# Performance work log

Hardware: AMD Instinct MI355X
Metric: run time of the kernel (lower is better)

The kernel has to match this reference:

```python
import jax, jax.numpy as jnp
import numpy as np

F = 128          # feature_size
C = 300          # n_content_dims
V = 100001       # n_nodes + 1 (embedding rows)
N0, N1, N2 = 409600, 40960, 4096   # NodeFlow layer sizes (fanout ~10)
E0, E1 = 409600, 40960             # edges in block0 (L0->L1) and block1 (L1->L2)


def setup_inputs() -> dict:
    key = jax.random.key(0)
    ks = jax.random.split(key, 24)
    std = 1.0 / F
    xav_p = float(np.sqrt(6.0 / (C + F)))   # xavier_uniform for proj Linear(C->F)
    xav_c = float(np.sqrt(6.0 / (2 * F + F)))  # xavier_uniform for conv Linear(2F->F)
    return {
        'nid0': jax.random.randint(ks[0], (N0,), 0, 100000),
        'nid1': jax.random.randint(ks[1], (N1,), 0, 100000),
        'nid2': jax.random.randint(ks[2], (N2,), 0, 100000),
        'content0': jax.random.normal(ks[3], (N0, C), jnp.float32),
        'content1': jax.random.normal(ks[4], (N1, C), jnp.float32),
        'content2': jax.random.normal(ks[5], (N2, C), jnp.float32),
        'block0_src': jax.random.randint(ks[6], (E0,), 0, N0),
        'block0_dst': jax.random.randint(ks[7], (E0,), 0, N1),
        'block1_src': jax.random.randint(ks[8], (E1,), 0, N1),
        'block1_dst': jax.random.randint(ks[9], (E1,), 0, N2),
        'node_emb': jax.random.normal(ks[10], (V, F), jnp.float32) * std,
        'Wp0': jax.random.uniform(ks[11], (F, C), jnp.float32, -xav_p, xav_p),
        'bp0': jnp.zeros((F,), jnp.float32),
        'Wp1': jax.random.uniform(ks[12], (F, C), jnp.float32, -xav_p, xav_p),
        'bp1': jnp.zeros((F,), jnp.float32),
        'Wp2': jax.random.uniform(ks[13], (F, C), jnp.float32, -xav_p, xav_p),
        'bp2': jnp.zeros((F,), jnp.float32),
        'Wc0': jax.random.uniform(ks[14], (F, 2 * F), jnp.float32, -xav_c, xav_c),
        'bc0': jnp.zeros((F,), jnp.float32),
        'Wc1': jax.random.uniform(ks[15], (F, 2 * F), jnp.float32, -xav_c, xav_c),
        'bc1': jnp.zeros((F,), jnp.float32),
    }


def _embed(node_emb, nid, content, Wp, bp):
    # h = node_emb(nid + 1) + LeakyReLU(content @ Wp.T + bp)   (dropout is eval no-op)
    return node_emb[nid + 1] + jax.nn.leaky_relu(content @ Wp.T + bp)


def _conv(h_src, src, dst, h_self, n_dst, W, b):
    # DGL block_compute: copy_src('h')+sum -> h_agg ; copy_src('one')+sum -> w
    msgs = h_src[src]                                    # [E, F] gather
    h_agg = jax.ops.segment_sum(msgs, dst, num_segments=n_dst)
    w = jax.ops.segment_sum(jnp.ones((src.shape[0],), h_src.dtype), dst,
                            num_segments=n_dst)
    h_agg = (h_agg - h_self) / jnp.maximum(w - 1.0, 1.0)[:, None]
    h_new = jax.nn.leaky_relu(jnp.concatenate([h_self, h_agg], axis=1) @ W.T + b)
    nrm = jnp.maximum(jnp.linalg.norm(h_new, axis=1, keepdims=True), 1e-6)
    return h_new / nrm


def reference(nid0, nid1, nid2, content0, content1, content2,
              block0_src, block0_dst, block1_src, block1_dst,
              node_emb, Wp0, bp0, Wp1, bp1, Wp2, bp2,
              Wc0, bc0, Wc1, bc1):
    h0 = _embed(node_emb, nid0, content0, Wp0, bp0)   # [N0, F]
    h1 = _embed(node_emb, nid1, content1, Wp1, bp1)   # [N1, F]
    h2 = _embed(node_emb, nid2, content2, Wp2, bp2)   # [N2, F]
    h1 = _conv(h0, block0_src, block0_dst, h1, N1, Wc0, bc0)
    h2 = _conv(h1, block1_src, block1_dst, h2, N2, Wc1, bc1)
    return h2
```

## Files before the change

kernel.cpp:

```cpp
#include <hip/hip_runtime.h>
#include <hip/hip_bf16.h>
#include <math.h>

#define F 128
#define C 300
#define CKP 320
#define NKT 10
#define K2F 256
#define N0_ 409600
#define N1_ 40960
#define N2_ 4096
#define E0_ 409600
#define E1_ 40960
#define CAP 64
#define LDA 40

typedef unsigned short u16;
typedef unsigned int u32;
typedef __attribute__((ext_vector_type(8))) short short8;
typedef __attribute__((ext_vector_type(8))) unsigned short u16x8;
typedef __attribute__((ext_vector_type(4))) float f32x4;

__device__ __forceinline__ float lrelu(float x) { return x > 0.f ? x : 0.01f * x; }

__device__ __forceinline__ u16 f2bf(float x) {
  __hip_bfloat16 h = __float2bfloat16(x);
  u16 r; __builtin_memcpy(&r, &h, 2); return r;
}
__device__ __forceinline__ float bf2f(u16 v) {
  union { u32 u; float f; } c; c.u = ((u32)v) << 16; return c.f;
}

#define GLOAD_LDS16(gp, lp) \
  __builtin_amdgcn_global_load_lds( \
      (const __attribute__((address_space(1))) void*)(const void*)(gp), \
      (__attribute__((address_space(3))) void*)(lp), 16, 0, 0)

__global__ __launch_bounds__(256) void zero_kernel(float4* __restrict__ p, int n4) {
  int i = blockIdx.x * 256 + threadIdx.x;
  if (i < n4) p[i] = make_float4(0.f, 0.f, 0.f, 0.f);
}

__global__ __launch_bounds__(256) void convert_all(
    const float* __restrict__ Wp0, const float* __restrict__ Wp1,
    const float* __restrict__ Wp2, const float* __restrict__ Wc0,
    const float* __restrict__ Wc1,
    u16* __restrict__ Wpb0, u16* __restrict__ Wpb1, u16* __restrict__ Wpb2,
    u16* __restrict__ Wcb0, u16* __restrict__ Wcb1)
{
  int i = blockIdx.x * 256 + threadIdx.x;
  const int P = F * CKP, Q = F * K2F;
  const float* W; u16* O; int K, KP, j;
  if      (i < P)         { W = Wp0; O = Wpb0; K = C;   KP = CKP; j = i; }
  else if (i < 2 * P)     { W = Wp1; O = Wpb1; K = C;   KP = CKP; j = i - P; }
  else if (i < 3 * P)     { W = Wp2; O = Wpb2; K = C;   KP = CKP; j = i - 2 * P; }
  else if (i < 3 * P + Q) { W = Wc0; O = Wcb0; K = K2F; KP = K2F; j = i - 3 * P; }
  else if (i < 3 * P + 2 * Q) { W = Wc1; O = Wcb1; K = K2F; KP = K2F; j = i - 3 * P - Q; }
  else return;
  int f = j / KP, k = j - f * KP;
  O[j] = (k < K) ? f2bf(W[(size_t)f * K + k]) : (u16)0;
}

__global__ __launch_bounds__(256) void build_csr(
    const int* __restrict__ b0s, const int* __restrict__ b0d,
    const int* __restrict__ b1s, const int* __restrict__ b1d,
    int* __restrict__ deg0, int* __restrict__ deg1,
    int* __restrict__ csr0, int* __restrict__ csr1)
{
  int e = blockIdx.x * 256 + threadIdx.x;
  if (e < E0_) {
    int d = b0d[e];
    int slot = atomicAdd(&deg0[d], 1);
    if (slot < CAP) csr0[(size_t)d * CAP + slot] = b0s[e];
  } else {
    int e1 = e - E0_;
    if (e1 < E1_) {
      int d = b1d[e1];
      int slot = atomicAdd(&deg1[d], 1);
      if (slot < CAP) csr1[(size_t)d * CAP + slot] = b1s[e1];
    }
  }
}

struct Afrag { float4 x00, x01, x10, x11; };

__global__ __launch_bounds__(256, 2) void embed_all(
    const float* __restrict__ content0, const float* __restrict__ content1,
    const float* __restrict__ content2,
    const u16* __restrict__ Wpb0, const u16* __restrict__ Wpb1,
    const u16* __restrict__ Wpb2,
    const float* __restrict__ bp0, const float* __restrict__ bp1,
    const float* __restrict__ bp2,
    const int* __restrict__ nid0, const int* __restrict__ nid1,
    const int* __restrict__ nid2,
    const float* __restrict__ emb,
    u16* __restrict__ out0, u16* __restrict__ out1, u16* __restrict__ out2)
{
  __shared__ u16 Bs[NKT * 128 * 32];
  const int t = threadIdx.x, lane = t & 63, w = t >> 6;
  const int b = blockIdx.x;

  const float* content; const u16* Wpb; const float* bp; const int* nid;
  u16* out; int ostride, row0;
  if (b < N0_ / 128) {
    content = content0; Wpb = Wpb0; bp = bp0; nid = nid0;
    out = out0; ostride = F; row0 = b * 128;
  } else if (b < N0_ / 128 + N1_ / 128) {
    content = content1; Wpb = Wpb1; bp = bp1; nid = nid1;
    out = out1; ostride = 2 * F; row0 = (b - N0_ / 128) * 128;
  } else {
    content = content2; Wpb = Wpb2; bp = bp2; nid = nid2;
    out = out2; ostride = 2 * F; row0 = (b - N0_ / 128 - N1_ / 128) * 128;
  }

  {
    const int j_in = lane >> 2, u_in = lane & 3;
#pragma unroll
    for (int cc = 0; cc < 20; ++cc) {
      int c = w * 20 + cc;
      int kt = c >> 3, j0 = (c & 7) * 16;
      int j = j0 + j_in;
      int u = u_in ^ (j & 3);
      const u16* gp = Wpb + (size_t)j * CKP + kt * 32 + u * 8;
      GLOAD_LDS16(gp, &Bs[(size_t)(kt * 128 + j0) * 32]);
    }
  }

  f32x4 acc[2][8];
#pragma unroll
  for (int fr = 0; fr < 2; ++fr)
#pragma unroll
    for (int fc = 0; fc < 8; ++fc) {
      acc[fr][fc][0] = 0.f; acc[fr][fc][1] = 0.f;
      acc[fr][fc][2] = 0.f; acc[fr][fc][3] = 0.f;
    }

  const int frow = lane & 15, g = lane >> 4;
  const float* c0p = content + (size_t)(row0 + w * 32 + frow) * C;
  const float* c1p = c0p + (size_t)16 * C;

  auto loadA = [&](int kt) -> Afrag {
    Afrag r;
    int col = kt * 32 + g * 8;
    if (kt < NKT - 1) {
      r.x00 = *(const float4*)(c0p + col); r.x01 = *(const float4*)(c0p + col + 4);
      r.x10 = *(const float4*)(c1p + col); r.x11 = *(const float4*)(c1p + col + 4);
    } else {
      float v0[8], v1[8];
#pragma unroll
      for (int i = 0; i < 8; ++i) {
        int cc = col + i;
        v0[i] = (cc < C) ? c0p[cc] : 0.f;
        v1[i] = (cc < C) ? c1p[cc] : 0.f;
      }
      r.x00 = make_float4(v0[0], v0[1], v0[2], v0[3]);
      r.x01 = make_float4(v0[4], v0[5], v0[6], v0[7]);
      r.x10 = make_float4(v1[0], v1[1], v1[2], v1[3]);
      r.x11 = make_float4(v1[4], v1[5], v1[6], v1[7]);
    }
    return r;
  };

  const int bsw = (g ^ (frow & 3)) * 8;
  auto compute = [&](const Afrag& a, int kt) {
    u16x8 a0v, a1v;
    a0v[0]=f2bf(a.x00.x); a0v[1]=f2bf(a.x00.y); a0v[2]=f2bf(a.x00.z); a0v[3]=f2bf(a.x00.w);
    a0v[4]=f2bf(a.x01.x); a0v[5]=f2bf(a.x01.y); a0v[6]=f2bf(a.x01.z); a0v[7]=f2bf(a.x01.w);
    a1v[0]=f2bf(a.x10.x); a1v[1]=f2bf(a.x10.y); a1v[2]=f2bf(a.x10.z); a1v[3]=f2bf(a.x10.w);
    a1v[4]=f2bf(a.x11.x); a1v[5]=f2bf(a.x11.y); a1v[6]=f2bf(a.x11.z); a1v[7]=f2bf(a.x11.w);
    short8 a0 = *(short8*)&a0v, a1 = *(short8*)&a1v;
#pragma unroll
    for (int fc = 0; fc < 8; ++fc) {
      short8 bfr = *(const short8*)&Bs[(size_t)(kt * 128 + fc * 16 + frow) * 32 + bsw];
      acc[0][fc] = __builtin_amdgcn_mfma_f32_16x16x32_bf16(a0, bfr, acc[0][fc], 0, 0, 0);
      acc[1][fc] = __builtin_amdgcn_mfma_f32_16x16x32_bf16(a1, bfr, acc[1][fc], 0, 0, 0);
    }
  };

  Afrag A0 = loadA(0);
  Afrag A1 = loadA(1);
  __syncthreads();
  Afrag A2 = loadA(2); compute(A0, 0);
  Afrag A3 = loadA(3); compute(A1, 1);
  A0 = loadA(4);       compute(A2, 2);
  A1 = loadA(5);       compute(A3, 3);
  A2 = loadA(6);       compute(A0, 4);
  A3 = loadA(7);       compute(A1, 5);
  A0 = loadA(8);       compute(A2, 6);
  A1 = loadA(9);       compute(A3, 7);
  compute(A0, 8);
  compute(A1, 9);

  float bpv[8];
#pragma unroll
  for (int fc = 0; fc < 8; ++fc) bpv[fc] = bp[fc * 16 + frow];
#pragma unroll
  for (int fr = 0; fr < 2; ++fr) {
#pragma unroll
    for (int q = 0; q < 4; ++q) {
      int n = row0 + w * 32 + fr * 16 + g * 4 + q;
      int gi = nid[n] + 1;
      const float* erow = emb + (size_t)gi * F;
      u16* orow = out + (size_t)n * ostride;
#pragma unroll
      for (int fc = 0; fc < 8; ++fc) {
        int col = fc * 16 + frow;
        float v = acc[fr][fc][q] + bpv[fc];
        orow[col] = f2bf(erow[col] + lrelu(v));
      }
    }
  }
}

__global__ __launch_bounds__(256) void gather_xa(
    const u16* __restrict__ hsrc, const int* __restrict__ csr,
    const int* __restrict__ deg, u16* __restrict__ xcat)
{
  int d = blockIdx.x * 4 + (threadIdx.x >> 6);
  int lane = threadIdx.x & 63;
  u32 hv = *(const u32*)&xcat[(size_t)d * (2 * F) + lane * 2];
  float h0f = bf2f((u16)(hv & 0xffff)), h1f = bf2f((u16)(hv >> 16));
  int dg = deg[d];
  int n = dg < CAP ? dg : CAP;
  const int* cp = csr + (size_t)d * CAP;
  float s0 = 0.f, s1 = 0.f;
  int j = 0;
  for (; j + 4 <= n; j += 4) {
    int i0 = cp[j], i1 = cp[j + 1], i2 = cp[j + 2], i3 = cp[j + 3];
    u32 v0 = *(const u32*)&hsrc[(size_t)i0 * F + lane * 2];
    u32 v1 = *(const u32*)&hsrc[(size_t)i1 * F + lane * 2];
    u32 v2 = *(const u32*)&hsrc[(size_t)i2 * F + lane * 2];
    u32 v3 = *(const u32*)&hsrc[(size_t)i3 * F + lane * 2];
    s0 += bf2f((u16)(v0 & 0xffff)) + bf2f((u16)(v1 & 0xffff))
        + bf2f((u16)(v2 & 0xffff)) + bf2f((u16)(v3 & 0xffff));
    s1 += bf2f((u16)(v0 >> 16)) + bf2f((u16)(v1 >> 16))
        + bf2f((u16)(v2 >> 16)) + bf2f((u16)(v3 >> 16));
  }
  for (; j < n; ++j) {
    u32 v = *(const u32*)&hsrc[(size_t)cp[j] * F + lane * 2];
    s0 += bf2f((u16)(v & 0xffff));
    s1 += bf2f((u16)(v >> 16));
  }
  float inv = 1.f / fmaxf((float)dg - 1.f, 1.f);
  u16 a0 = f2bf((s0 - h0f) * inv), a1 = f2bf((s1 - h1f) * inv);
  *(u32*)&xcat[(size_t)d * (2 * F) + F + lane * 2] = ((u32)a1 << 16) | a0;
}

template<int F32OUT>
__global__ __launch_bounds__(256) void conv_mfma(
    const u16* __restrict__ xcat, const u16* __restrict__ Wcb,
    const float* __restrict__ bc, u16* __restrict__ outb,
    float* __restrict__ outf)
{
  __shared__ u16 As[128][LDA];
  __shared__ u16 Bs[128][LDA];
  const int t = threadIdx.x;
  const int lane = t & 63, w = t >> 6;
  const int row0 = blockIdx.x * 128;

  f32x4 acc[2][8];
#pragma unroll
  for (int fr = 0; fr < 2; ++fr)
#pragma unroll
    for (int fc = 0; fc < 8; ++fc) {
      acc[fr][fc][0] = 0.f; acc[fr][fc][1] = 0.f;
      acc[fr][fc][2] = 0.f; acc[fr][fc][3] = 0.f;
    }

  for (int k0 = 0; k0 < K2F; k0 += 32) {
    if (k0) __syncthreads();
#pragma unroll
    for (int it = 0; it < 2; ++it) {
      int cc = it * 256 + t;
      int r = cc >> 2, kc = (cc & 3) * 8;
      *(u16x8*)&As[r][kc] = *(const u16x8*)&xcat[(size_t)(row0 + r) * K2F + k0 + kc];
      *(u16x8*)&Bs[r][kc] = *(const u16x8*)&Wcb[(size_t)r * K2F + k0 + kc];
    }
    __syncthreads();

    const int frow = lane & 15;
    const int kc = (lane >> 4) * 8;
    short8 a0 = *(const short8*)&As[w * 32 + frow][kc];
    short8 a1 = *(const short8*)&As[w * 32 + 16 + frow][kc];
#pragma unroll
    for (int fc = 0; fc < 8; ++fc) {
      short8 b = *(const short8*)&Bs[fc * 16 + frow][kc];
      acc[0][fc] = __builtin_amdgcn_mfma_f32_16x16x32_bf16(a0, b, acc[0][fc], 0, 0, 0);
      acc[1][fc] = __builtin_amdgcn_mfma_f32_16x16x32_bf16(a1, b, acc[1][fc], 0, 0, 0);
    }
  }

  float bcv[8];
#pragma unroll
  for (int fc = 0; fc < 8; ++fc) bcv[fc] = bc[fc * 16 + (lane & 15)];
#pragma unroll
  for (int fr = 0; fr < 2; ++fr) {
#pragma unroll
    for (int q = 0; q < 4; ++q) {
      float x[8];
      float ss = 0.f;
#pragma unroll
      for (int fc = 0; fc < 8; ++fc) {
        x[fc] = lrelu(acc[fr][fc][q] + bcv[fc]);
        ss += x[fc] * x[fc];
      }
#pragma unroll
      for (int m = 8; m >= 1; m >>= 1) ss += __shfl_xor(ss, m, 64);
      float nrm = 1.f / fmaxf(sqrtf(ss), 1e-6f);
      int n = row0 + w * 32 + fr * 16 + (lane >> 4) * 4 + q;
#pragma unroll
      for (int fc = 0; fc < 8; ++fc) {
        int col = fc * 16 + (lane & 15);
        if (F32OUT) outf[(size_t)n * F + col] = x[fc] * nrm;
        else        outb[(size_t)n * F + col] = f2bf(x[fc] * nrm);
      }
    }
  }
}

extern "C" void kernel_launch(void* const* d_in, const int* in_sizes, int n_in,
                              void* d_out, int out_size, void* d_ws, size_t ws_size,
                              hipStream_t stream) {
  const int*   nid0     = (const int*)d_in[0];
  const int*   nid1     = (const int*)d_in[1];
  const int*   nid2     = (const int*)d_in[2];
  const float* content0 = (const float*)d_in[3];
  const float* content1 = (const float*)d_in[4];
  const float* content2 = (const float*)d_in[5];
  const int*   b0s      = (const int*)d_in[6];
  const int*   b0d      = (const int*)d_in[7];
  const int*   b1s      = (const int*)d_in[8];
  const int*   b1d      = (const int*)d_in[9];
  const float* emb      = (const float*)d_in[10];
  const float* Wp0      = (const float*)d_in[11];
  const float* bp0      = (const float*)d_in[12];
  const float* Wp1      = (const float*)d_in[13];
  const float* bp1      = (const float*)d_in[14];
  const float* Wp2      = (const float*)d_in[15];
  const float* bp2      = (const float*)d_in[16];
  const float* Wc0      = (const float*)d_in[17];
  const float* bc0      = (const float*)d_in[18];
  const float* Wc1      = (const float*)d_in[19];
  const float* bc1      = (const float*)d_in[20];

  u16* wsu = (u16*)d_ws;
  u16* h0b   = wsu;
  u16* xcat1 = h0b + (size_t)N0_ * F;
  u16* xcat2 = xcat1 + (size_t)N1_ * 2 * F;
  u16* h1nb  = xcat2 + (size_t)N2_ * 2 * F;
  u16* Wpb0  = h1nb + (size_t)N1_ * F;
  u16* Wpb1  = Wpb0 + (size_t)F * CKP;
  u16* Wpb2  = Wpb1 + (size_t)F * CKP;
  u16* Wcb0  = Wpb2 + (size_t)F * CKP;
  u16* Wcb1  = Wcb0 + (size_t)F * K2F;
  int* deg0  = (int*)(Wcb1 + (size_t)F * K2F);
  int* deg1  = deg0 + N1_;
  int* csr0  = deg1 + N2_;
  int* csr1  = csr0 + (size_t)N1_ * CAP;

  const int zn4 = (N1_ + N2_) / 4;
  zero_kernel<<<(zn4 + 255) / 256, 256, 0, stream>>>((float4*)deg0, zn4);

  build_csr<<<(E0_ + E1_ + 255) / 256, 256, 0, stream>>>(
      b0s, b0d, b1s, b1d, deg0, deg1, csr0, csr1);

  convert_all<<<(3 * F * CKP + 2 * F * K2F + 255) / 256, 256, 0, stream>>>(
      Wp0, Wp1, Wp2, Wc0, Wc1, Wpb0, Wpb1, Wpb2, Wcb0, Wcb1);

  embed_all<<<(N0_ + N1_ + N2_) / 128, 256, 0, stream>>>(
      content0, content1, content2, Wpb0, Wpb1, Wpb2,
      bp0, bp1, bp2, nid0, nid1, nid2, emb, h0b, xcat1, xcat2);

  gather_xa<<<N1_ / 4, 256, 0, stream>>>(h0b, csr0, deg0, xcat1);
  conv_mfma<0><<<N1_ / 128, 256, 0, stream>>>(xcat1, Wcb0, bc0, h1nb, nullptr);

  gather_xa<<<N2_ / 4, 256, 0, stream>>>(h1nb, csr1, deg1, xcat2);
  conv_mfma<1><<<N2_ / 128, 256, 0, stream>>>(xcat2, Wcb1, bc1, nullptr, (float*)d_out);
}
```

Measured before the change: 321.6 us.

## Make embed GEMM persistent with per-wave double-buffered coalesced panel loads

The embed kernel becomes a persistent grid of 256 blocks, with each wave looping over 16-row panels in strided order. Each panel is loaded with fully coalesced float4 reads of contiguous content rows into a register double buffer. It is then converted to bf16 and staged in a per-wave LDS tile before the MFMA k-loop. This loads the projection weights into LDS once per block instead of once per 128 rows and improves global read coalescing. In exchange it uses heavy register buffering (38 float4 per lane), one block per CU, and a per-wave LDS write/read round trip with no explicit wave barrier.

```diff
diff --git a/kernel.cpp b/kernel.cpp
--- a/kernel.cpp
+++ b/kernel.cpp
@@ -14,9 +14,18 @@
 #define E1_ 40960
 #define CAP 64
 #define LDA 40
+#define ALD 328
+
+#define NB0 230
+#define NB1 23
+#define NB2 3
+#define NP0 (N0_ / 16)
+#define NP1 (N1_ / 16)
+#define NP2 (N2_ / 16)
 
 typedef unsigned short u16;
 typedef unsigned int u32;
+typedef __attribute__((ext_vector_type(2))) unsigned int u32x2;
 typedef __attribute__((ext_vector_type(8))) short short8;
 typedef __attribute__((ext_vector_type(8))) unsigned short u16x8;
 typedef __attribute__((ext_vector_type(4))) float f32x4;
@@ -82,9 +91,7 @@
   }
 }
 
-struct Afrag { float4 x00, x01, x10, x11; };
-
-__global__ __launch_bounds__(256, 2) void embed_all(
+__global__ __launch_bounds__(256, 1) void embed_all(
     const float* __restrict__ content0, const float* __restrict__ content1,
     const float* __restrict__ content2,
     const u16* __restrict__ Wpb0, const u16* __restrict__ Wpb1,
@@ -97,20 +104,21 @@
     u16* __restrict__ out0, u16* __restrict__ out1, u16* __restrict__ out2)
 {
   __shared__ u16 Bs[NKT * 128 * 32];
+  __shared__ u16 As[4][16][ALD];
   const int t = threadIdx.x, lane = t & 63, w = t >> 6;
   const int b = blockIdx.x;
 
   const float* content; const u16* Wpb; const float* bp; const int* nid;
-  u16* out; int ostride, row0;
-  if (b < N0_ / 128) {
+  u16* out; int ostride, npan, wstr, bl;
+  if (b < NB0) {
     content = content0; Wpb = Wpb0; bp = bp0; nid = nid0;
-    out = out0; ostride = F; row0 = b * 128;
-  } else if (b < N0_ / 128 + N1_ / 128) {
+    out = out0; ostride = F;     npan = NP0; wstr = NB0 * 4; bl = b;
+  } else if (b < NB0 + NB1) {
     content = content1; Wpb = Wpb1; bp = bp1; nid = nid1;
-    out = out1; ostride = 2 * F; row0 = (b - N0_ / 128) * 128;
+    out = out1; ostride = 2 * F; npan = NP1; wstr = NB1 * 4; bl = b - NB0;
   } else {
     content = content2; Wpb = Wpb2; bp = bp2; nid = nid2;
-    out = out2; ostride = 2 * F; row0 = (b - N0_ / 128 - N1_ / 128) * 128;
+    out = out2; ostride = 2 * F; npan = NP2; wstr = NB2 * 4; bl = b - NB0 - NB1;
   }
 
   {
@@ -126,89 +134,91 @@
     }
   }
 
-  f32x4 acc[2][8];
-#pragma unroll
-  for (int fr = 0; fr < 2; ++fr)
+#pragma unroll
+  for (int j = 0; j < 3; ++j) {
+    int idx = j * 64 + lane;
+    if (idx < 160) {
+      int r = idx / 10, kk = 300 + (idx % 10) * 2;
+      *(u32*)&As[w][r][kk] = 0u;
+    }
+  }
+
+  const int frow = lane & 15, g = lane >> 4;
+  const int bsw = (g ^ (frow & 3)) * 8;
+  float bpv[8];
+#pragma unroll
+  for (int fc = 0; fc < 8; ++fc) bpv[fc] = bp[fc * 16 + frow];
+
+  f32x4 acc[8];
+
+  auto loadP = [&](float4* buf, int pl) {
+    const float* ab = content + (size_t)pl * 16 * C;
+#pragma unroll
+    for (int i = 0; i < 19; ++i) {
+      int c = i * 64 + lane;
+      if (c < 1200) buf[i] = *(const float4*)(ab + (size_t)c * 4);
+      else buf[i] = make_float4(0.f, 0.f, 0.f, 0.f);
+    }
+  };
+  auto cvtWrite = [&](const float4* buf) {
+#pragma unroll
+    for (int i = 0; i < 19; ++i) {
+      int c = i * 64 + lane;
+      if (c < 1200) {
+        int r = c / 75, k0 = (c % 75) * 4;
+        u32 lo = ((u32)f2bf(buf[i].y) << 16) | f2bf(buf[i].x);
+        u32 hi = ((u32)f2bf(buf[i].w) << 16) | f2bf(buf[i].z);
+        u32x2 pk; pk[0] = lo; pk[1] = hi;
+        *(u32x2*)&As[w][r][k0] = pk;
+      }
+    }
+  };
+  auto kloop = [&]() {
 #pragma unroll
     for (int fc = 0; fc < 8; ++fc) {
-      acc[fr][fc][0] = 0.f; acc[fr][fc][1] = 0.f;
-      acc[fr][fc][2] = 0.f; acc[fr][fc][3] = 0.f;
-    }
-
-  const int frow = lane & 15, g = lane >> 4;
-  const float* c0p = content + (size_t)(row0 + w * 32 + frow) * C;
-  const float* c1p = c0p + (size_t)16 * C;
-
-  auto loadA = [&](int kt) -> Afrag {
-    Afrag r;
-    int col = kt * 32 + g * 8;
-    if (kt < NKT - 1) {
-      r.x00 = *(const float4*)(c0p + col); r.x01 = *(const float4*)(c0p + col + 4);
-      r.x10 = *(const float4*)(c1p + col); r.x11 = *(const float4*)(c1p + col + 4);
-    } else {
-      float v0[8], v1[8];
-#pragma unroll
-      for (int i = 0; i < 8; ++i) {
-        int cc = col + i;
-        v0[i] = (cc < C) ? c0p[cc] : 0.f;
-        v1[i] = (cc < C) ? c1p[cc] : 0.f;
-      }
-      r.x00 = make_float4(v0[0], v0[1], v0[2], v0[3]);
-      r.x01 = make_float4(v0[4], v0[5], v0[6], v0[7]);
-      r.x10 = make_float4(v1[0], v1[1], v1[2], v1[3]);
-      r.x11 = make_float4(v1[4], v1[5], v1[6], v1[7]);
-    }
-    return r;
+      acc[fc][0] = 0.f; acc[fc][1] = 0.f; acc[fc][2] = 0.f; acc[fc][3] = 0.f;
+    }
+#pragma unroll
+    for (int kt = 0; kt < NKT; ++kt) {
+      short8 a = *(const short8*)&As[w][frow][kt * 32 + g * 8];
+#pragma unroll
+      for (int fc = 0; fc < 8; ++fc) {
+        short8 bfr = *(const short8*)&Bs[(size_t)(kt * 128 + fc * 16 + frow) * 32 + bsw];
+        acc[fc] = __builtin_amdgcn_mfma_f32_16x16x32_bf16(a, bfr, acc[fc], 0, 0, 0);
+      }
+    }
   };
-
-  const int bsw = (g ^ (frow & 3)) * 8;
-  auto compute = [&](const Afrag& a, int kt) {
-    u16x8 a0v, a1v;
-    a0v[0]=f2bf(a.x00.x); a0v[1]=f2bf(a.x00.y); a0v[2]=f2bf(a.x00.z); a0v[3]=f2bf(a.x00.w);
-    a0v[4]=f2bf(a.x01.x); a0v[5]=f2bf(a.x01.y); a0v[6]=f2bf(a.x01.z); a0v[7]=f2bf(a.x01.w);
-    a1v[0]=f2bf(a.x10.x); a1v[1]=f2bf(a.x10.y); a1v[2]=f2bf(a.x10.z); a1v[3]=f2bf(a.x10.w);
-    a1v[4]=f2bf(a.x11.x); a1v[5]=f2bf(a.x11.y); a1v[6]=f2bf(a.x11.z); a1v[7]=f2bf(a.x11.w);
-    short8 a0 = *(short8*)&a0v, a1 = *(short8*)&a1v;
-#pragma unroll
-    for (int fc = 0; fc < 8; ++fc) {
-      short8 bfr = *(const short8*)&Bs[(size_t)(kt * 128 + fc * 16 + frow) * 32 + bsw];
-      acc[0][fc] = __builtin_amdgcn_mfma_f32_16x16x32_bf16(a0, bfr, acc[0][fc], 0, 0, 0);
-      acc[1][fc] = __builtin_amdgcn_mfma_f32_16x16x32_bf16(a1, bfr, acc[1][fc], 0, 0, 0);
-    }
-  };
-
-  Afrag A0 = loadA(0);
-  Afrag A1 = loadA(1);
-  __syncthreads();
-  Afrag A2 = loadA(2); compute(A0, 0);
-  Afrag A3 = loadA(3); compute(A1, 1);
-  A0 = loadA(4);       compute(A2, 2);
-  A1 = loadA(5);       compute(A3, 3);
-  A2 = loadA(6);       compute(A0, 4);
-  A3 = loadA(7);       compute(A1, 5);
-  A0 = loadA(8);       compute(A2, 6);
-  A1 = loadA(9);       compute(A3, 7);
-  compute(A0, 8);
-  compute(A1, 9);
-
-  float bpv[8];
-#pragma unroll
-  for (int fc = 0; fc < 8; ++fc) bpv[fc] = bp[fc * 16 + frow];
-#pragma unroll
-  for (int fr = 0; fr < 2; ++fr) {
+  auto epi = [&](int pl) {
 #pragma unroll
     for (int q = 0; q < 4; ++q) {
-      int n = row0 + w * 32 + fr * 16 + g * 4 + q;
+      int n = pl * 16 + g * 4 + q;
       int gi = nid[n] + 1;
       const float* erow = emb + (size_t)gi * F;
       u16* orow = out + (size_t)n * ostride;
 #pragma unroll
       for (int fc = 0; fc < 8; ++fc) {
         int col = fc * 16 + frow;
-        float v = acc[fr][fc][q] + bpv[fc];
-        orow[col] = f2bf(erow[col] + lrelu(v));
-      }
-    }
+        orow[col] = f2bf(erow[col] + lrelu(acc[fc][q] + bpv[fc]));
+      }
+    }
+  };
+
+  float4 bufA[19], bufB[19];
+  int p = bl * 4 + w;
+  loadP(bufA, p);
+  __syncthreads();
+
+  while (true) {
+    int p2 = p + wstr;
+    loadP(bufB, (p2 < npan) ? p2 : p);
+    cvtWrite(bufA); kloop(); epi(p);
+    if (p2 >= npan) break;
+    p = p2;
+    int p3 = p + wstr;
+    loadP(bufA, (p3 < npan) ? p3 : p);
+    cvtWrite(bufB); kloop(); epi(p);
+    if (p3 >= npan) break;
+    p = p3;
   }
 }
 
@@ -367,7 +377,7 @@
   convert_all<<<(3 * F * CKP + 2 * F * K2F + 255) / 256, 256, 0, stream>>>(
       Wp0, Wp1, Wp2, Wc0, Wc1, Wpb0, Wpb1, Wpb2, Wcb0, Wcb1);
 
-  embed_all<<<(N0_ + N1_ + N2_) / 128, 256, 0, stream>>>(
+  embed_all<<<NB0 + NB1 + NB2, 256, 0, stream>>>(
       content0, content1, content2, Wpb0, Wpb1, Wpb2,
       bp0, bp1, bp2, nid0, nid1, nid2, emb, h0b, xcat1, xcat2);
 
```

Result: slower. 475.9 us (+48.0%).
